# Performance work log

Hardware: AMD Instinct MI355X
Metric: run time of the kernel (lower is better)

## Reference

```python
import jax, jax.numpy as jnp
import numpy as np

B, T, HID = 1, 2048, 2048
H, KVH, D = 32, 8, 64
G = H // KVH          # kv groups = 4
SCALE = 1.0 / np.sqrt(D)
NEG = -1e9


def _rotate_half(x):
    x1, x2 = x[..., : D // 2], x[..., D // 2 :]
    return jnp.concatenate((-x2, x1), axis=-1)


def setup_inputs() -> dict:
    key = jax.random.key(0)
    ks = jax.random.split(key, 8)
    hidden_states = jax.random.normal(ks[0], (B, T, HID), jnp.float32)
    # RoPE tables (faithful shapes; realistic values)
    pos = jnp.arange(T, dtype=jnp.float32)[:, None]
    inv = 1.0 / (10000.0 ** (jnp.arange(0, D, 2, dtype=jnp.float32) / D))
    ang = pos * inv[None, :]                      # [T, D/2]
    ang = jnp.concatenate([ang, ang], axis=-1)    # [T, D]
    cos = jnp.broadcast_to(jnp.cos(ang)[None], (B, T, D))
    sin = jnp.broadcast_to(jnp.sin(ang)[None], (B, T, D))
    # causal additive mask [B,1,T,T]
    causal = jnp.tril(jnp.ones((T, T), bool))
    attention_mask_4d = jnp.where(causal, 0.0, NEG).astype(jnp.float32)[None, None]
    s = 0.02
    Wq = jax.random.normal(ks[1], (H * D, HID), jnp.float32) * s
    Wk = jax.random.normal(ks[2], (KVH * D, HID), jnp.float32) * s
    Wv = jax.random.normal(ks[3], (KVH * D, HID), jnp.float32) * s
    Wo = jax.random.normal(ks[4], (HID, H * D), jnp.float32) * s
    return {"hidden_states": hidden_states, "cos": cos, "sin": sin,
            "attention_mask_4d": attention_mask_4d,
            "Wq": Wq, "Wk": Wk, "Wv": Wv, "Wo": Wo}


def reference(hidden_states, cos, sin, attention_mask_4d, Wq, Wk, Wv, Wo):
    x = hidden_states
    b, t, _ = x.shape
    # QKV projections (nn.Linear: x @ W.T), then [B, heads, T, D]
    q = (x @ Wq.T).reshape(b, t, H, D).transpose(0, 2, 1, 3)
    k = (x @ Wk.T).reshape(b, t, KVH, D).transpose(0, 2, 1, 3)
    v = (x @ Wv.T).reshape(b, t, KVH, D).transpose(0, 2, 1, 3)
    # rotary: cos/sin [B,T,D] -> broadcast over heads
    c = cos[:, None]; s = sin[:, None]
    q = q * c + _rotate_half(q) * s
    k = k * c + _rotate_half(k) * s
    # grouped-query attention with fp32 scores/softmax
    qg = q.reshape(b, KVH, G, t, D)
    scores = jnp.einsum('bkgtd,bksd->bkgts', qg.astype(jnp.float32),
                        k.astype(jnp.float32)) * SCALE
    m = attention_mask_4d[:, 0].astype(jnp.float32)  # [B,T,S]
    scores = scores + m[:, None, None, :, :]
    probs = jax.nn.softmax(scores, axis=-1)
    out = jnp.einsum('bkgts,bksd->bkgtd', probs.astype(v.dtype), v)
    out = out.astype(q.dtype).reshape(b, H, t, D)
    out = out.transpose(0, 2, 1, 3).reshape(b, t, H * D)
    return out @ Wo.T
```

## Files before the change

kernel.cpp:

```cpp
#include <hip/hip_runtime.h>
#include <math.h>

typedef __attribute__((ext_vector_type(8))) __bf16 bf16x8;
typedef __attribute__((ext_vector_type(4))) float  f32x4;
typedef unsigned short ushort_t;
typedef unsigned int   uint_t;

static __device__ inline f32x4 mfma16(bf16x8 a, bf16x8 b, f32x4 c) {
    return __builtin_amdgcn_mfma_f32_16x16x32_bf16(a, b, c, 0, 0, 0);
}

static __device__ inline ushort_t f2b(float f) {
    uint_t u = __builtin_bit_cast(uint_t, f);
    u = (u + 0x7FFFu + ((u >> 16) & 1u)) >> 16;
    return (ushort_t)u;
}
static __device__ inline float b2f(ushort_t u) {
    uint_t x = ((uint_t)u) << 16;
    return __builtin_bit_cast(float, x);
}
static __device__ inline bf16x8 ld8(const ushort_t* p) {
    uint4 v = *(const uint4*)p;
    return __builtin_bit_cast(bf16x8, v);
}
static __device__ inline float fexp2(float x) {
#if __has_builtin(__builtin_amdgcn_exp2f)
    return __builtin_amdgcn_exp2f(x);
#else
    return exp2f(x);
#endif
}

static __device__ inline void gl_lds16(const ushort_t* g, ushort_t* l) {
    __builtin_amdgcn_global_load_lds(
        (const __attribute__((address_space(1))) void*)(g),
        (__attribute__((address_space(3))) void*)(l),
        16, 0, 0);
}

#define WS_XB     0
#define WS_WQKV   8388608
#define WS_WO     20971520
#define WS_P0     29360128
#define WS_QBB    0
#define WS_KBB    8388608
#define WS_VTG    10485760
#define WS_AB     12582912

__global__ __launch_bounds__(256) void cvt_all(const float* __restrict__ x,
                                               const float* __restrict__ wq,
                                               const float* __restrict__ wk,
                                               const float* __restrict__ wv,
                                               const float* __restrict__ wo,
                                               ushort_t* __restrict__ dst) {
    const size_t i = (size_t)(blockIdx.x * 256 + threadIdx.x) * 4;
    const float* src; size_t off;
    if (i < 4194304)       { src = x;  off = 0; }
    else if (i < 8388608)  { src = wq; off = 4194304; }
    else if (i < 9437184)  { src = wk; off = 8388608; }
    else if (i < 10485760) { src = wv; off = 9437184; }
    else                   { src = wo; off = 10485760; }
    float4 v = *(const float4*)(src + (i - off));
    ushort4 o;
    o.x = f2b(v.x); o.y = f2b(v.y); o.z = f2b(v.z); o.w = f2b(v.w);
    *(ushort4*)(dst + i) = o;
}

__global__ __launch_bounds__(512, 2) void gemm_fk(const ushort_t* __restrict__ A,
                                                  const ushort_t* __restrict__ Bt,
                                                  ushort_t* __restrict__ Cout,
                                                  int N, int K) {
    __shared__ ushort_t lds[49152];
    const int tid  = threadIdx.x;
    const int lane = tid & 63, w = tid >> 6;
    const int qn = lane & 15, quad = lane >> 4;
    const long m0 = (long)blockIdx.y * 256;
    const long n0 = (long)blockIdx.x * 128;
    const int NT = K >> 6;
    ushort_t* ldsp = lds;

    const int srow = w * 8 + (lane >> 3);
    const int scol = ((lane & 7) ^ (lane >> 3)) * 8;
    const ushort_t* gA = A + (m0 + srow) * (size_t)K + scol;
    const int srB  = tid >> 3;
    const int scB  = ((tid & 7) ^ (srB & 7)) * 8;
    const ushort_t* gB = Bt + (n0 + srB) * (size_t)K + scB;

    const int wm = w >> 1, wn = w & 1;
    const int aRow = (wm * 32 + qn) * 64;
    const int bRow = (wn * 32 + qn) * 64;
    const int sw0 = ((quad * 16)      ^ ((qn & 7) << 4)) >> 1;
    const int sw1 = ((64 + quad * 16) ^ ((qn & 7) << 4)) >> 1;

#define KSTG_A(t, h, buf)                                                      \
    do { if ((t) < NT) {                                                       \
        const ushort_t* g = gA + (size_t)(h) * 128 * K + (t) * 64;             \
        ushort_t* d = ldsp + (buf) * 24576 + (h) * 8192 + w * 512;             \
        gl_lds16(g, d);                                                        \
        gl_lds16(g + 64 * (size_t)K, d + 4096);                                \
    } } while (0)
#define KSTG_B(t, h, buf)                                                      \
    do { if ((t) < NT) {                                                       \
        const ushort_t* g = gB + (size_t)(h) * 64 * K + (t) * 64;              \
        ushort_t* d = ldsp + (buf) * 24576 + 16384 + (h) * 4096 + w * 512;     \
        gl_lds16(g, d);                                                        \
    } } while (0)

#define KPHASE(cb, p, qr, qc, STAGE, BOUND)                                    \
    do {                                                                       \
        const ushort_t* bA = ldsp + (cb) * 24576 + (qr) * 8192;                \
        const ushort_t* bB = ldsp + (cb) * 24576 + 16384 + (qc) * 4096;        \
        bf16x8 af[2][2], bv[2][2];                                             \
        _Pragma("unroll")                                                      \
        for (int mi = 0; mi < 2; mi++) {                                       \
            af[mi][0] = *(const bf16x8*)(bA + aRow + mi * 1024 + sw0);         \
            af[mi][1] = *(const bf16x8*)(bA + aRow + mi * 1024 + sw1);         \
        }                                                                      \
        _Pragma("unroll")                                                      \
        for (int nj = 0; nj < 2; nj++) {                                       \
            bv[nj][0] = *(const bf16x8*)(bB + bRow + nj * 1024 + sw0);         \
            bv[nj][1] = *(const bf16x8*)(bB + bRow + nj * 1024 + sw1);         \
        }                                                                      \
        asm volatile("" ::: "memory");                                         \
        STAGE;                                                                 \
        BOUND;                                                                 \
        __builtin_amdgcn_s_barrier();                                          \
        asm volatile("s_waitcnt lgkmcnt(0)" ::: "memory");                     \
        __builtin_amdgcn_sched_barrier(0);                                     \
        __builtin_amdgcn_s_setprio(1);                                         \
        _Pragma("unroll")                                                      \
        for (int mi = 0; mi < 2; mi++)                                         \
            _Pragma("unroll")                                                  \
            for (int nj = 0; nj < 2; nj++) {                                   \
                acc[p][mi][nj] = mfma16(af[mi][0], bv[nj][0], acc[p][mi][nj]); \
                acc[p][mi][nj] = mfma16(af[mi][1], bv[nj][1], acc[p][mi][nj]); \
            }                                                                  \
        __builtin_amdgcn_s_setprio(0);                                         \
        __builtin_amdgcn_s_barrier();                                          \
    } while (0)

    f32x4 acc[4][2][2];
    f32x4 zero = {0.f, 0.f, 0.f, 0.f};
    #pragma unroll
    for (int p = 0; p < 4; p++)
        #pragma unroll
        for (int mi = 0; mi < 2; mi++)
            #pragma unroll
            for (int nj = 0; nj < 2; nj++) acc[p][mi][nj] = zero;

    KSTG_A(0, 0, 0); KSTG_B(0, 0, 0); KSTG_B(0, 1, 0); KSTG_A(0, 1, 0);
    KSTG_A(1, 0, 1); KSTG_B(1, 0, 1);
    asm volatile("s_waitcnt vmcnt(0)" ::: "memory");
    __builtin_amdgcn_s_barrier();

    for (int t2 = 0; t2 < NT; t2 += 2) {
        KPHASE(0, 0, 0, 0, KSTG_B(t2 + 1, 1, 1), (void)0);
        KPHASE(0, 1, 0, 1, KSTG_A(t2 + 1, 1, 1), (void)0);
        KPHASE(0, 2, 1, 0, KSTG_A(t2 + 2, 0, 0), (void)0);
        KPHASE(0, 3, 1, 1, KSTG_B(t2 + 2, 0, 0),
               if (t2 == NT - 2) { asm volatile("s_waitcnt vmcnt(0)" ::: "memory"); }
               else              { asm volatile("s_waitcnt vmcnt(3)" ::: "memory"); });
        KPHASE(1, 0, 0, 0, KSTG_B(t2 + 2, 1, 0), (void)0);
        KPHASE(1, 1, 0, 1, KSTG_A(t2 + 2, 1, 0), (void)0);
        KPHASE(1, 2, 1, 0, KSTG_A(t2 + 3, 0, 1), (void)0);
        KPHASE(1, 3, 1, 1, KSTG_B(t2 + 3, 0, 1),
               asm volatile("s_waitcnt vmcnt(3)" ::: "memory"););
    }
#undef KPHASE
#undef KSTG_A
#undef KSTG_B

    #pragma unroll
    for (int p = 0; p < 4; p++) {
        const int qr = p >> 1, qc = p & 1;
        #pragma unroll
        for (int mi = 0; mi < 2; mi++)
            #pragma unroll
            for (int nj = 0; nj < 2; nj++) {
                const long row0 = m0 + qr * 128 + wm * 32 + mi * 16 + quad * 4;
                const long col  = n0 + qc * 64 + wn * 32 + nj * 16 + qn;
                #pragma unroll
                for (int r = 0; r < 4; r++)
                    Cout[(row0 + r) * N + col] = f2b(acc[p][mi][nj][r]);
            }
    }
}

__global__ __launch_bounds__(512, 2) void gemm_on(const ushort_t* __restrict__ A,
                                                  const ushort_t* __restrict__ Bt,
                                                  float* __restrict__ Cout,
                                                  int N, int K) {
    __shared__ ushort_t lds[40960];
    const int tid  = threadIdx.x;
    const int lane = tid & 63, w = tid >> 6;
    const int qn = lane & 15, quad = lane >> 4;
    const long m0 = (long)blockIdx.y * 256;
    const long n0 = (long)blockIdx.x * 64;
    const int NT = K >> 6;
    ushort_t* ldsp = lds;

    const int srow = w * 8 + (lane >> 3);
    const int scol = ((lane & 7) ^ (lane >> 3)) * 8;
    const ushort_t* gA = A + (m0 + srow) * (size_t)K + scol;
    const int srB  = tid >> 3;
    const int scB  = ((tid & 7) ^ (srB & 7)) * 8;
    const ushort_t* gB = Bt + (n0 + srB) * (size_t)K + scB;

    const int wm = w >> 1, wn = w & 1;
    const int aRow = (wm * 32 + qn) * 64;
    const int bRow = (wn * 32 + qn) * 64;
    const int sw0 = ((quad * 16)      ^ ((qn & 7) << 4)) >> 1;
    const int sw1 = ((64 + quad * 16) ^ ((qn & 7) << 4)) >> 1;

#define NSTG_A(t, h, buf)                                                      \
    do { if ((t) < NT) {                                                       \
        const ushort_t* g = gA + (size_t)(h) * 128 * K + (t) * 64;             \
        ushort_t* d = ldsp + (buf) * 20480 + (h) * 8192 + w * 512;             \
        gl_lds16(g, d);                                                        \
        gl_lds16(g + 64 * (size_t)K, d + 4096);                                \
    } } while (0)
#define NSTG_B(t, buf)                                                         \
    do { if ((t) < NT) {                                                       \
        const ushort_t* g = gB + (size_t)(t) * 64;                             \
        ushort_t* d = ldsp + (buf) * 20480 + 16384 + w * 512;                  \
        gl_lds16(g, d);                                                        \
    } } while (0)

#define NPHASE(cb, qr, STAGE, BOUND)                                           \
    do {                                                                       \
        const ushort_t* bA = ldsp + (cb) * 20480 + (qr) * 8192;                \
        const ushort_t* bB = ldsp + (cb) * 20480 + 16384;                      \
        bf16x8 af[2][2], bv[2][2];                                             \
        _Pragma("unroll")                                                      \
        for (int mi = 0; mi < 2; mi++) {                                       \
            af[mi][0] = *(const bf16x8*)(bA + aRow + mi * 1024 + sw0);         \
            af[mi][1] = *(const bf16x8*)(bA + aRow + mi * 1024 + sw1);         \
        }                                                                      \
        _Pragma("unroll")                                                      \
        for (int nj = 0; nj < 2; nj++) {                                       \
            bv[nj][0] = *(const bf16x8*)(bB + bRow + nj * 1024 + sw0);         \
            bv[nj][1] = *(const bf16x8*)(bB + bRow + nj * 1024 + sw1);         \
        }                                                                      \
        asm volatile("" ::: "memory");                                         \
        STAGE;                                                                 \
        BOUND;                                                                 \
        __builtin_amdgcn_s_barrier();                                          \
        asm volatile("s_waitcnt lgkmcnt(0)" ::: "memory");                     \
        __builtin_amdgcn_sched_barrier(0);                                     \
        __builtin_amdgcn_s_setprio(1);                                         \
        _Pragma("unroll")                                                      \
        for (int mi = 0; mi < 2; mi++)                                         \
            _Pragma("unroll")                                                  \
            for (int nj = 0; nj < 2; nj++) {                                   \
                acc[qr][mi][nj] = mfma16(af[mi][0], bv[nj][0], acc[qr][mi][nj]); \
                acc[qr][mi][nj] = mfma16(af[mi][1], bv[nj][1], acc[qr][mi][nj]); \
            }                                                                  \
        __builtin_amdgcn_s_setprio(0);                                         \
        __builtin_amdgcn_s_barrier();                                          \
    } while (0)

    f32x4 acc[2][2][2];
    f32x4 zero = {0.f, 0.f, 0.f, 0.f};
    #pragma unroll
    for (int p = 0; p < 2; p++)
        #pragma unroll
        for (int mi = 0; mi < 2; mi++)
            #pragma unroll
            for (int nj = 0; nj < 2; nj++) acc[p][mi][nj] = zero;

    NSTG_A(0, 0, 0); NSTG_A(0, 1, 0); NSTG_B(0, 0);
    NSTG_A(1, 0, 1);
    asm volatile("s_waitcnt vmcnt(0)" ::: "memory");
    __builtin_amdgcn_s_barrier();

    for (int t = 0; t < NT; t++) {
        const int cb = t & 1;
        NPHASE(cb, 0, { NSTG_A(t + 1, 1, cb ^ 1); NSTG_B(t + 1, cb ^ 1); },
               (void)0);
        NPHASE(cb, 1, { NSTG_A(t + 2, 0, cb); },
               if (t == NT - 2) { asm volatile("s_waitcnt vmcnt(0)" ::: "memory"); }
               else             { asm volatile("s_waitcnt vmcnt(2)" ::: "memory"); });
    }
#undef NPHASE
#undef NSTG_A
#undef NSTG_B

    #pragma unroll
    for (int p = 0; p < 2; p++)
        #pragma unroll
        for (int mi = 0; mi < 2; mi++)
            #pragma unroll
            for (int nj = 0; nj < 2; nj++) {
                const long row0 = m0 + p * 128 + wm * 32 + mi * 16 + quad * 4;
                const long col  = n0 + wn * 32 + nj * 16 + qn;
                #pragma unroll
                for (int r = 0; r < 4; r++)
                    Cout[(row0 + r) * N + col] = acc[p][mi][nj][r];
            }
}

__global__ __launch_bounds__(256) void fuse_crv(const ushort_t* __restrict__ p0,
                                                const float* __restrict__ cs,
                                                const float* __restrict__ sn,
                                                ushort_t* __restrict__ qd,
                                                ushort_t* __restrict__ kd,
                                                ushort_t* __restrict__ vt) {
    __shared__ ushort_t tl[64][65];
    const int cx = blockIdx.x;
    const int ty = blockIdx.y;
    const int r  = threadIdx.x >> 2;
    const int c0 = (threadIdx.x & 3) << 4;
    const int t  = ty * 64 + r;
    const size_t base = (size_t)t * 3072 + cx * 64;

    if (cx < 40) {
        const int cp = c0 ^ 32;
        float own[16], par[16];
        #pragma unroll
        for (int jj = 0; jj < 2; jj++) {
            uint4 a = *(const uint4*)(p0 + base + c0 + jj * 8);
            uint4 c = *(const uint4*)(p0 + base + cp + jj * 8);
            const ushort_t* pa = (const ushort_t*)&a;
            const ushort_t* pc = (const ushort_t*)&c;
            #pragma unroll
            for (int e = 0; e < 8; e++) {
                own[jj * 8 + e] = b2f(pa[e]);
                par[jj * 8 + e] = b2f(pc[e]);
            }
        }
        float cs16[16], sn16[16];
        #pragma unroll
        for (int jj = 0; jj < 4; jj++) {
            float4 c4 = *(const float4*)(cs + (size_t)t * 64 + c0 + jj * 4);
            float4 s4 = *(const float4*)(sn + (size_t)t * 64 + c0 + jj * 4);
            cs16[jj * 4 + 0] = c4.x; cs16[jj * 4 + 1] = c4.y;
            cs16[jj * 4 + 2] = c4.z; cs16[jj * 4 + 3] = c4.w;
            sn16[jj * 4 + 0] = s4.x; sn16[jj * 4 + 1] = s4.y;
            sn16[jj * 4 + 2] = s4.z; sn16[jj * 4 + 3] = s4.w;
        }
        const float scale = (cx < 32) ? 0.18033688f : 1.0f;
        union { ushort_t u[16]; uint4 v[2]; } o;
        #pragma unroll
        for (int j = 0; j < 16; j++) {
            const int d = c0 + j;
            const float pr = (d < 32) ? -par[j] : par[j];
            o.u[j] = f2b((own[j] * cs16[j] + pr * sn16[j]) * scale);
        }
        if (cx < 32) {
            ushort_t* dst = qd + (size_t)t * 2048 + cx * 64 + c0;
            *(uint4*)dst = o.v[0]; *(uint4*)(dst + 8) = o.v[1];
        } else {
            ushort_t* dst = kd + (size_t)t * 512 + (cx - 32) * 64 + c0;
            *(uint4*)dst = o.v[0]; *(uint4*)(dst + 8) = o.v[1];
        }
    } else {
        #pragma unroll
        for (int jj = 0; jj < 2; jj++) {
            uint4 a = *(const uint4*)(p0 + base + c0 + jj * 8);
            const ushort_t* pa = (const ushort_t*)&a;
            #pragma unroll
            for (int e = 0; e < 8; e++)
                tl[r][c0 + jj * 8 + e] = pa[e];
        }
        __syncthreads();
        const int rr  = threadIdx.x >> 3;
        const int cc8 = (threadIdx.x & 7) * 8;
        const int db = (cx - 40) * 64, tb = ty * 64;
        #pragma unroll
        for (int h = 0; h < 2; h++) {
            const int d = rr + h * 32;
            ushort4 o0, o1;
            o0.x = tl[cc8 + 0][d]; o0.y = tl[cc8 + 1][d];
            o0.z = tl[cc8 + 2][d]; o0.w = tl[cc8 + 3][d];
            o1.x = tl[cc8 + 4][d]; o1.y = tl[cc8 + 5][d];
            o1.z = tl[cc8 + 6][d]; o1.w = tl[cc8 + 7][d];
            *(ushort4*)(vt + (size_t)(db + d) * 2048 + tb + cc8)     = o0;
            *(ushort4*)(vt + (size_t)(db + d) * 2048 + tb + cc8 + 4) = o1;
        }
    }
}

__global__ __launch_bounds__(256) void attn_kernel(const ushort_t* __restrict__ Q,
                                                   const ushort_t* __restrict__ Kb,
                                                   const ushort_t* __restrict__ Vt,
                                                   ushort_t* __restrict__ Ob) {
    __shared__ ushort_t Ks[2 * 4096];
    __shared__ ushort_t Vs[2 * 4096];
    __shared__ ushort_t pl[4 * 16 * 72];
    const int tid  = threadIdx.x;
    const int lane = tid & 63, wid = tid >> 6;
    const int qn = lane & 15, quad = lane >> 4;
    const int h   = blockIdx.x & 31;
    const int qb  = 31 - (blockIdx.x >> 5);
    const int kvb = (h >> 2) * 64;
    const int trow = qb * 64 + wid * 16;
    ushort_t* plw = pl + wid * 16 * 72;
    f32x4 zero = {0.f, 0.f, 0.f, 0.f};

    const ushort_t* qpA = Q + (size_t)(trow + qn) * 2048 + h * 64 + quad * 8;
    const bf16x8 qA0 = ld8(qpA), qA1 = ld8(qpA + 32);

    f32x4 oA[4] = {zero, zero, zero, zero};
    float lsum = 0.f;
    const int ntiles = qb + 1;

#define STAGE(s0, buf)                                                         \
    do {                                                                       \
        const ushort_t* kg = Kb + (size_t)((s0) + lane) * 512 + kvb + wid * 8; \
        gl_lds16(kg,      Ks + (buf) * 4096 + wid * 512);                      \
        gl_lds16(kg + 32, Ks + (buf) * 4096 + (wid + 4) * 512);                \
        const ushort_t* vg = Vt + (size_t)(kvb + lane) * 2048 + (s0) + wid * 8;\
        gl_lds16(vg,      Vs + (buf) * 4096 + wid * 512);                      \
        gl_lds16(vg + 32, Vs + (buf) * 4096 + (wid + 4) * 512);                \
    } while (0)

#define COMPUTE(s0, buf)                                                       \
    do {                                                                       \
        f32x4 scA[4];                                                          \
        __builtin_amdgcn_s_setprio(1);                                         \
        _Pragma("unroll")                                                      \
        for (int cb = 0; cb < 4; cb++) {                                       \
            const bf16x8 kf0 = *(const bf16x8*)(Ks + (buf) * 4096 + quad * 512 + (cb * 16 + qn) * 8);       \
            const bf16x8 kf1 = *(const bf16x8*)(Ks + (buf) * 4096 + (quad + 4) * 512 + (cb * 16 + qn) * 8); \
            f32x4 s = mfma16(kf0, qA0, zero); scA[cb] = mfma16(kf1, qA1, s);   \
        }                                                                      \
        __builtin_amdgcn_s_setprio(0);                                         \
        const bool needmask = ((s0) + 63 > trow);                              \
        const int tA = trow + qn;                                              \
        _Pragma("unroll")                                                      \
        for (int cb = 0; cb < 4; cb++) {                                       \
            float pv0, pv1, pv2, pv3;                                          \
            {                                                                  \
                const int colb = (s0) + cb * 16 + quad * 4;                    \
                float v0 = scA[cb][0], v1 = scA[cb][1];                        \
                float v2 = scA[cb][2], v3 = scA[cb][3];                        \
                if (needmask) {                                                \
                    if (colb + 0 > tA) v0 = -INFINITY;                         \
                    if (colb + 1 > tA) v1 = -INFINITY;                         \
                    if (colb + 2 > tA) v2 = -INFINITY;                         \
                    if (colb + 3 > tA) v3 = -INFINITY;                         \
                }                                                              \
                pv0 = fexp2(v0); pv1 = fexp2(v1);                              \
                pv2 = fexp2(v2); pv3 = fexp2(v3);                              \
            }                                                                  \
            lsum += pv0 + pv1 + pv2 + pv3;                                     \
            uint_t w0, w1;                                                     \
            asm("v_cvt_pk_bf16_f32 %0, %1, %2" : "=v"(w0) : "v"(pv0), "v"(pv1)); \
            asm("v_cvt_pk_bf16_f32 %0, %1, %2" : "=v"(w1) : "v"(pv2), "v"(pv3)); \
            uint2 pk; pk.x = w0; pk.y = w1;                                    \
            *(uint2*)(plw + qn * 72 + cb * 16 + quad * 4) = pk;                \
        }                                                                      \
        const bf16x8 pfA0 = *(const bf16x8*)(plw + qn * 72 + quad * 8);        \
        const bf16x8 pfA1 = *(const bf16x8*)(plw + qn * 72 + 32 + quad * 8);   \
        __builtin_amdgcn_s_setprio(1);                                         \
        _Pragma("unroll")                                                      \
        for (int dcb = 0; dcb < 4; dcb++) {                                    \
            const bf16x8 vf0 = *(const bf16x8*)(Vs + (buf) * 4096 + quad * 512 + (dcb * 16 + qn) * 8);       \
            const bf16x8 vf1 = *(const bf16x8*)(Vs + (buf) * 4096 + (quad + 4) * 512 + (dcb * 16 + qn) * 8); \
            oA[dcb] = mfma16(pfA0, vf0, oA[dcb]);                              \
            oA[dcb] = mfma16(pfA1, vf1, oA[dcb]);                              \
        }                                                                      \
        __builtin_amdgcn_s_setprio(0);                                         \
    } while (0)

    STAGE(0, 0);
    int t = 0;
    for (; t + 2 <= ntiles; t += 2) {
        __syncthreads();
        STAGE((t + 1) * 64, 1);
        COMPUTE(t * 64, 0);
        __syncthreads();
        if (t + 2 < ntiles) STAGE((t + 2) * 64, 0);
        COMPUTE((t + 1) * 64, 1);
    }
    if (t < ntiles) {
        __syncthreads();
        COMPUTE(t * 64, 0);
    }
#undef STAGE
#undef COMPUTE

    float sA = lsum;
    sA += __shfl_xor(sA, 16, 64);
    sA += __shfl_xor(sA, 32, 64);
    #pragma unroll
    for (int i = 0; i < 4; i++) {
        const float invA = 1.0f / __shfl(sA, quad * 4 + i, 64);
        ushort_t* obA = Ob + (size_t)(trow + quad * 4 + i) * 2048 + h * 64 + qn;
        obA[0]  = f2b(oA[0][i] * invA);
        obA[16] = f2b(oA[1][i] * invA);
        obA[32] = f2b(oA[2][i] * invA);
        obA[48] = f2b(oA[3][i] * invA);
    }
}

extern "C" void kernel_launch(void* const* d_in, const int* in_sizes, int n_in,
                              void* d_out, int out_size, void* d_ws, size_t ws_size,
                              hipStream_t stream) {
    const float* x    = (const float*)d_in[0];
    const float* cosp = (const float*)d_in[1];
    const float* sinp = (const float*)d_in[2];
    const float* Wq = (const float*)d_in[4];
    const float* Wk = (const float*)d_in[5];
    const float* Wv = (const float*)d_in[6];
    const float* Wo = (const float*)d_in[7];
    char* ws = (char*)d_ws;
    (void)ws_size; (void)in_sizes; (void)n_in; (void)out_size;

    ushort_t* xb    = (ushort_t*)(ws + WS_XB);
    ushort_t* wqkvb = (ushort_t*)(ws + WS_WQKV);
    ushort_t* wob   = (ushort_t*)(ws + WS_WO);
    ushort_t* p0    = (ushort_t*)(ws + WS_P0);
    ushort_t* qbb   = (ushort_t*)(ws + WS_QBB);
    ushort_t* kbb   = (ushort_t*)(ws + WS_KBB);
    ushort_t* vtg   = (ushort_t*)(ws + WS_VTG);
    ushort_t* ab    = (ushort_t*)(ws + WS_AB);

    cvt_all<<<14336, 256, 0, stream>>>(x, Wq, Wk, Wv, Wo, xb);

    gemm_fk<<<dim3(24, 8), 512, 0, stream>>>(xb, wqkvb, p0, 3072, 2048);

    fuse_crv<<<dim3(48, 32), 256, 0, stream>>>(p0, cosp, sinp, qbb, kbb, vtg);

    attn_kernel<<<1024, 256, 0, stream>>>(qbb, kbb, vtg, ab);

    gemm_on<<<dim3(32, 8), 512, 0, stream>>>(ab, wob, (float*)d_out, 2048, 2048);
}
```

Measured before the change: 238.3 us.

## Fuse RoPE, Q scaling and V transpose into QKV GEMM epilogue

Removes the separate fuse_crv kernel and the intermediate bf16 QKV buffer by applying rotary embedding, the softmax scale, and the V transpose directly in the QKV GEMM epilogue. The warp tiling changes from 2x2 (32x32 per warp) to 1x4 (16 rows by a full 64-column head), so each lane holds both rotate-half partners in registers. This saves one launch and a full round trip of the projection output through memory. In exchange, A-fragment reuse across warps drops, epilogue stores are scattered 2-byte writes, and the workspace layout is reshuffled.

```diff
diff --git a/kernel.cpp b/kernel.cpp
--- a/kernel.cpp
+++ b/kernel.cpp
@@ -40,12 +40,11 @@
 
 #define WS_XB     0
 #define WS_WQKV   8388608
+#define WS_AB     12582912
 #define WS_WO     20971520
-#define WS_P0     29360128
-#define WS_QBB    0
-#define WS_KBB    8388608
-#define WS_VTG    10485760
-#define WS_AB     12582912
+#define WS_QBB    29360128
+#define WS_KBB    37748736
+#define WS_VTG    39845888
 
 __global__ __launch_bounds__(256) void cvt_all(const float* __restrict__ x,
                                                const float* __restrict__ wq,
@@ -66,10 +65,14 @@
     *(ushort4*)(dst + i) = o;
 }
 
-__global__ __launch_bounds__(512, 2) void gemm_fk(const ushort_t* __restrict__ A,
-                                                  const ushort_t* __restrict__ Bt,
-                                                  ushort_t* __restrict__ Cout,
-                                                  int N, int K) {
+__global__ __launch_bounds__(512, 2) void gemm_fkr(const ushort_t* __restrict__ A,
+                                                   const ushort_t* __restrict__ Bt,
+                                                   const float* __restrict__ cs,
+                                                   const float* __restrict__ sn,
+                                                   ushort_t* __restrict__ qd,
+                                                   ushort_t* __restrict__ kd,
+                                                   ushort_t* __restrict__ vt,
+                                                   int N, int K) {
     __shared__ ushort_t lds[49152];
     const int tid  = threadIdx.x;
     const int lane = tid & 63, w = tid >> 6;
@@ -86,9 +89,8 @@
     const int scB  = ((tid & 7) ^ (srB & 7)) * 8;
     const ushort_t* gB = Bt + (n0 + srB) * (size_t)K + scB;
 
-    const int wm = w >> 1, wn = w & 1;
-    const int aRow = (wm * 32 + qn) * 64;
-    const int bRow = (wn * 32 + qn) * 64;
+    const int aRow = (w * 16 + qn) * 64;
+    const int bRow = qn * 64;
     const int sw0 = ((quad * 16)      ^ ((qn & 7) << 4)) >> 1;
     const int sw1 = ((64 + quad * 16) ^ ((qn & 7) << 4)) >> 1;
 
@@ -110,14 +112,11 @@
     do {                                                                       \
         const ushort_t* bA = ldsp + (cb) * 24576 + (qr) * 8192;                \
         const ushort_t* bB = ldsp + (cb) * 24576 + 16384 + (qc) * 4096;        \
-        bf16x8 af[2][2], bv[2][2];                                             \
-        _Pragma("unroll")                                                      \
-        for (int mi = 0; mi < 2; mi++) {                                       \
-            af[mi][0] = *(const bf16x8*)(bA + aRow + mi * 1024 + sw0);         \
-            af[mi][1] = *(const bf16x8*)(bA + aRow + mi * 1024 + sw1);         \
-        }                                                                      \
-        _Pragma("unroll")                                                      \
-        for (int nj = 0; nj < 2; nj++) {                                       \
+        bf16x8 af[2], bv[4][2];                                                \
+        af[0] = *(const bf16x8*)(bA + aRow + sw0);                             \
+        af[1] = *(const bf16x8*)(bA + aRow + sw1);                             \
+        _Pragma("unroll")                                                      \
+        for (int nj = 0; nj < 4; nj++) {                                       \
             bv[nj][0] = *(const bf16x8*)(bB + bRow + nj * 1024 + sw0);         \
             bv[nj][1] = *(const bf16x8*)(bB + bRow + nj * 1024 + sw1);         \
         }                                                                      \
@@ -129,24 +128,20 @@
         __builtin_amdgcn_sched_barrier(0);                                     \
         __builtin_amdgcn_s_setprio(1);                                         \
         _Pragma("unroll")                                                      \
-        for (int mi = 0; mi < 2; mi++)                                         \
-            _Pragma("unroll")                                                  \
-            for (int nj = 0; nj < 2; nj++) {                                   \
-                acc[p][mi][nj] = mfma16(af[mi][0], bv[nj][0], acc[p][mi][nj]); \
-                acc[p][mi][nj] = mfma16(af[mi][1], bv[nj][1], acc[p][mi][nj]); \
-            }                                                                  \
+        for (int nj = 0; nj < 4; nj++) {                                       \
+            acc[p][nj] = mfma16(af[0], bv[nj][0], acc[p][nj]);                 \
+            acc[p][nj] = mfma16(af[1], bv[nj][1], acc[p][nj]);                 \
+        }                                                                      \
         __builtin_amdgcn_s_setprio(0);                                         \
         __builtin_amdgcn_s_barrier();                                          \
     } while (0)
 
-    f32x4 acc[4][2][2];
+    f32x4 acc[4][4];
     f32x4 zero = {0.f, 0.f, 0.f, 0.f};
     #pragma unroll
     for (int p = 0; p < 4; p++)
         #pragma unroll
-        for (int mi = 0; mi < 2; mi++)
-            #pragma unroll
-            for (int nj = 0; nj < 2; nj++) acc[p][mi][nj] = zero;
+        for (int nj = 0; nj < 4; nj++) acc[p][nj] = zero;
 
     KSTG_A(0, 0, 0); KSTG_B(0, 0, 0); KSTG_B(0, 1, 0); KSTG_A(0, 1, 0);
     KSTG_A(1, 0, 1); KSTG_B(1, 0, 1);
@@ -170,19 +165,47 @@
 #undef KSTG_A
 #undef KSTG_B
 
-    #pragma unroll
-    for (int p = 0; p < 4; p++) {
-        const int qr = p >> 1, qc = p & 1;
+    const int bx = blockIdx.x;
+    if (bx >= 20) {
         #pragma unroll
-        for (int mi = 0; mi < 2; mi++)
+        for (int p = 0; p < 4; p++) {
+            const int qr = p >> 1, qc = p & 1;
+            const long row0 = m0 + qr * 128 + w * 16 + quad * 4;
             #pragma unroll
-            for (int nj = 0; nj < 2; nj++) {
-                const long row0 = m0 + qr * 128 + wm * 32 + mi * 16 + quad * 4;
-                const long col  = n0 + qc * 64 + wn * 32 + nj * 16 + qn;
+            for (int nj = 0; nj < 4; nj++) {
+                const long c = (long)(bx - 20) * 128 + qc * 64 + nj * 16 + qn;
+                ushort4 o;
+                o.x = f2b(acc[p][nj][0]); o.y = f2b(acc[p][nj][1]);
+                o.z = f2b(acc[p][nj][2]); o.w = f2b(acc[p][nj][3]);
+                *(ushort4*)(vt + c * 2048 + row0) = o;
+            }
+        }
+    } else {
+        const bool isq = (bx < 16);
+        const float scale = isq ? 0.18033688f : 1.0f;
+        #pragma unroll
+        for (int p = 0; p < 4; p++) {
+            const int qr = p >> 1, qc = p & 1;
+            #pragma unroll
+            for (int r = 0; r < 4; r++) {
+                const long row = m0 + qr * 128 + w * 16 + quad * 4 + r;
+                const float* cr = cs + row * 64;
+                const float* sr = sn + row * 64;
                 #pragma unroll
-                for (int r = 0; r < 4; r++)
-                    Cout[(row0 + r) * N + col] = f2b(acc[p][mi][nj][r]);
+                for (int nj = 0; nj < 4; nj++) {
+                    const int d = nj * 16 + qn;
+                    const float own = acc[p][nj][r];
+                    const float par = acc[p][nj ^ 2][r];
+                    const float pr  = (d < 32) ? -par : par;
+                    const float val = (own * cr[d] + pr * sr[d]) * scale;
+                    const long col = (long)bx * 128 + qc * 64 + d;
+                    if (isq)
+                        qd[row * 2048 + col] = f2b(val);
+                    else
+                        kd[row * 512 + (col - 2048)] = f2b(val);
+                }
             }
+        }
     }
 }
 
@@ -297,87 +320,6 @@
                 for (int r = 0; r < 4; r++)
                     Cout[(row0 + r) * N + col] = acc[p][mi][nj][r];
             }
-}
-
-__global__ __launch_bounds__(256) void fuse_crv(const ushort_t* __restrict__ p0,
-                                                const float* __restrict__ cs,
-                                                const float* __restrict__ sn,
-                                                ushort_t* __restrict__ qd,
-                                                ushort_t* __restrict__ kd,
-                                                ushort_t* __restrict__ vt) {
-    __shared__ ushort_t tl[64][65];
-    const int cx = blockIdx.x;
-    const int ty = blockIdx.y;
-    const int r  = threadIdx.x >> 2;
-    const int c0 = (threadIdx.x & 3) << 4;
-    const int t  = ty * 64 + r;
-    const size_t base = (size_t)t * 3072 + cx * 64;
-
-    if (cx < 40) {
-        const int cp = c0 ^ 32;
-        float own[16], par[16];
-        #pragma unroll
-        for (int jj = 0; jj < 2; jj++) {
-            uint4 a = *(const uint4*)(p0 + base + c0 + jj * 8);
-            uint4 c = *(const uint4*)(p0 + base + cp + jj * 8);
-            const ushort_t* pa = (const ushort_t*)&a;
-            const ushort_t* pc = (const ushort_t*)&c;
-            #pragma unroll
-            for (int e = 0; e < 8; e++) {
-                own[jj * 8 + e] = b2f(pa[e]);
-                par[jj * 8 + e] = b2f(pc[e]);
-            }
-        }
-        float cs16[16], sn16[16];
-        #pragma unroll
-        for (int jj = 0; jj < 4; jj++) {
-            float4 c4 = *(const float4*)(cs + (size_t)t * 64 + c0 + jj * 4);
-            float4 s4 = *(const float4*)(sn + (size_t)t * 64 + c0 + jj * 4);
-            cs16[jj * 4 + 0] = c4.x; cs16[jj * 4 + 1] = c4.y;
-            cs16[jj * 4 + 2] = c4.z; cs16[jj * 4 + 3] = c4.w;
-            sn16[jj * 4 + 0] = s4.x; sn16[jj * 4 + 1] = s4.y;
-            sn16[jj * 4 + 2] = s4.z; sn16[jj * 4 + 3] = s4.w;
-        }
-        const float scale = (cx < 32) ? 0.18033688f : 1.0f;
-        union { ushort_t u[16]; uint4 v[2]; } o;
-        #pragma unroll
-        for (int j = 0; j < 16; j++) {
-            const int d = c0 + j;
-            const float pr = (d < 32) ? -par[j] : par[j];
-            o.u[j] = f2b((own[j] * cs16[j] + pr * sn16[j]) * scale);
-        }
-        if (cx < 32) {
-            ushort_t* dst = qd + (size_t)t * 2048 + cx * 64 + c0;
-            *(uint4*)dst = o.v[0]; *(uint4*)(dst + 8) = o.v[1];
-        } else {
-            ushort_t* dst = kd + (size_t)t * 512 + (cx - 32) * 64 + c0;
-            *(uint4*)dst = o.v[0]; *(uint4*)(dst + 8) = o.v[1];
-        }
-    } else {
-        #pragma unroll
-        for (int jj = 0; jj < 2; jj++) {
-            uint4 a = *(const uint4*)(p0 + base + c0 + jj * 8);
-            const ushort_t* pa = (const ushort_t*)&a;
-            #pragma unroll
-            for (int e = 0; e < 8; e++)
-                tl[r][c0 + jj * 8 + e] = pa[e];
-        }
-        __syncthreads();
-        const int rr  = threadIdx.x >> 3;
-        const int cc8 = (threadIdx.x & 7) * 8;
-        const int db = (cx - 40) * 64, tb = ty * 64;
-        #pragma unroll
-        for (int h = 0; h < 2; h++) {
-            const int d = rr + h * 32;
-            ushort4 o0, o1;
-            o0.x = tl[cc8 + 0][d]; o0.y = tl[cc8 + 1][d];
-            o0.z = tl[cc8 + 2][d]; o0.w = tl[cc8 + 3][d];
-            o1.x = tl[cc8 + 4][d]; o1.y = tl[cc8 + 5][d];
-            o1.z = tl[cc8 + 6][d]; o1.w = tl[cc8 + 7][d];
-            *(ushort4*)(vt + (size_t)(db + d) * 2048 + tb + cc8)     = o0;
-            *(ushort4*)(vt + (size_t)(db + d) * 2048 + tb + cc8 + 4) = o1;
-        }
-    }
 }
 
 __global__ __launch_bounds__(256) void attn_kernel(const ushort_t* __restrict__ Q,
@@ -510,7 +452,6 @@
     ushort_t* xb    = (ushort_t*)(ws + WS_XB);
     ushort_t* wqkvb = (ushort_t*)(ws + WS_WQKV);
     ushort_t* wob   = (ushort_t*)(ws + WS_WO);
-    ushort_t* p0    = (ushort_t*)(ws + WS_P0);
     ushort_t* qbb   = (ushort_t*)(ws + WS_QBB);
     ushort_t* kbb   = (ushort_t*)(ws + WS_KBB);
     ushort_t* vtg   = (ushort_t*)(ws + WS_VTG);
@@ -518,9 +459,8 @@
 
     cvt_all<<<14336, 256, 0, stream>>>(x, Wq, Wk, Wv, Wo, xb);
 
-    gemm_fk<<<dim3(24, 8), 512, 0, stream>>>(xb, wqkvb, p0, 3072, 2048);
-
-    fuse_crv<<<dim3(48, 32), 256, 0, stream>>>(p0, cosp, sinp, qbb, kbb, vtg);
+    gemm_fkr<<<dim3(24, 8), 512, 0, stream>>>(xb, wqkvb, cosp, sinp,
+                                              qbb, kbb, vtg, 3072, 2048);
 
     attn_kernel<<<1024, 256, 0, stream>>>(qbb, kbb, vtg, ab);
 
```

Result: no change. 240.5 us (+0.9%).
